# Optimization experiments

Measured on AMD Instinct MI355X. Metric: run time of the kernel, lower is better.

Reference implementation:

```python
import jax, jax.numpy as jnp
import numpy as np

TOP_K = 10


def setup_inputs() -> dict:
    key = jax.random.key(0)
    x = jax.random.normal(key, (256, 1, 8192), dtype=jnp.float32)
    return {"x": x}


def reference(x):
    # x: [B, 1, S] real
    B, _, S = x.shape
    # torch.arange(1e-05, 1, 1/S) has exactly S elements for these S
    t = 1e-05 + jnp.arange(S, dtype=jnp.float32) / S            # [S]
    dft = jnp.fft.fft(x[:, 0, :], n=S, axis=-1, norm='ortho')   # [B, S] complex64
    mag = jnp.abs(dft)                                          # [B, S]
    top_idx = jnp.argsort(-mag, axis=-1)[:, :TOP_K]             # [B, k] int
    top_dft = jnp.take_along_axis(dft, top_idx, axis=1)         # [B, k] complex
    # complex exponential basis exp(-2j*pi*k*t), flipped along time
    phase = (-2j * jnp.pi) * (top_idx[:, :, None].astype(jnp.float32) * t[None, None, :])
    bs = jnp.exp(phase)[:, :, ::-1]                             # [B, k, S] complex
    bf = top_dft[:, :, None] * bs / jnp.sqrt(jnp.float32(S))    # [B, k, S]
    # F.pad((1,0), mode='replicate') then crop to S: shift right by 1, duplicate first col
    bf = jnp.concatenate([bf[:, :, :1], bf[:, :, :-1]], axis=-1)
    bf = bf[:, :, None, :]                                      # [B, k, 1, S]
    residual = x - jnp.sum(bf, axis=1)                          # [B, 1, S] complex
    return bf, residual
```

## Files before the change

### kernel.cpp

```cpp
#include <hip/hip_runtime.h>

#define NB    256
#define SLEN  8192
#define LOG2S 13
#define TOPK  10

#define RES_REAL   ((size_t)20971520)
#define FULL_ILV   ((size_t)46137344)

__device__ __forceinline__ float sin_rev(float p) { return __builtin_amdgcn_sinf(p); }
__device__ __forceinline__ float cos_rev(float p) { return __builtin_amdgcn_cosf(p); }

__device__ __forceinline__ bool beats(float om, int oi, float wm, int wi) {
  return (om > wm * 1.0001f) || (om > wm * 0.9999f && oi < wi);
}

__global__ __launch_bounds__(512, 1)
void fourier_fused(const float* __restrict__ x, float* __restrict__ out, size_t cap) {
  __shared__ float re[SLEN];
  __shared__ float im[SLEN];

  const int b = blockIdx.x;
  const int t = threadIdx.x;
  const int lane = t & 63;
  const int wid  = t >> 6;
  const float* xb = x + (size_t)b * SLEN;

  for (int i = t; i < SLEN; i += 512) { re[i] = xb[i]; im[i] = 0.f; }
  __syncthreads();

  for (int i = t; i < SLEN; i += 512) {
    int j = (int)(__brev((unsigned)i) >> (32 - LOG2S));
    if (i < j) { float tmp = re[i]; re[i] = re[j]; re[j] = tmp; }
  }
  __syncthreads();

  for (int stage = 1; stage <= LOG2S; ++stage) {
    const int half = 1 << (stage - 1);
    const float invm = 1.f / (float)(1 << stage);
    for (int bfi = t; bfi < SLEN / 2; bfi += 512) {
      const int pos = bfi & (half - 1);
      const int i = ((bfi >> (stage - 1)) << stage) + pos;
      const int j = i + half;
      const float p = (float)pos * invm;
      const float c  = cos_rev(p);
      const float sn = -sin_rev(p);
      const float vr = re[j], vi = im[j];
      const float tr = vr * c - vi * sn;
      const float ti = vr * sn + vi * c;
      const float ur = re[i], ui = im[i];
      re[i] = ur + tr; im[i] = ui + ti;
      re[j] = ur - tr; im[j] = ui - ti;
    }
    __syncthreads();
  }

  int   kk[TOPK];
  float ar[TOPK], ai[TOPK];
#pragma unroll
  for (int sel = 0; sel < TOPK; ++sel) {
    float wm = -1.f; int wi = SLEN;
    for (int i = t; i < SLEN; i += 512) {
      const float m2 = re[i] * re[i] + im[i] * im[i];
      if (m2 > wm * 1.0001f) { wm = m2; wi = i; }
    }
    for (int off = 32; off > 0; off >>= 1) {
      const float om = __shfl_down(wm, off);
      const int   oi = __shfl_down(wi, off);
      if (beats(om, oi, wm, wi)) { wm = om; wi = oi; }
    }
    __syncthreads();
    float sv_r = 0.f, sv_i = 0.f;
    if (t < 8) { sv_r = re[t]; sv_i = im[t]; }
    __syncthreads();
    if (lane == 0) { re[wid] = wm; im[wid] = __int_as_float(wi); }
    __syncthreads();
    wm = re[0]; wi = __float_as_int(im[0]);
    for (int w = 1; w < 8; ++w) {
      const float om = re[w]; const int oi = __float_as_int(im[w]);
      if (beats(om, oi, wm, wi)) { wm = om; wi = oi; }
    }
    __syncthreads();
    if (t < 8) { re[t] = sv_r; im[t] = sv_i; }
    __syncthreads();
    const float rr = re[wi] * (1.f / (float)SLEN);
    const float ii = im[wi] * (1.f / (float)SLEN);
    const float pr = -1e-5f * (float)wi;
    const float cp = cos_rev(pr), sp = sin_rev(pr);
    kk[sel] = wi;
    ar[sel] = rr * cp - ii * sp;
    ai[sel] = rr * sp + ii * cp;
    __syncthreads();
    if (t == 0) { re[wi] = 0.f; im[wi] = 0.f; }
    __syncthreads();
  }

  if (cap < FULL_ILV) {
    const size_t bfbase = (size_t)b * TOPK * SLEN;
    for (int pass = 0; pass < 4; ++pass) {
      const int s0 = pass * 2048 + t * 4;
      const float4 xv = *(const float4*)(xb + s0);
      float acc0 = 0.f, acc1 = 0.f, acc2 = 0.f, acc3 = 0.f;
#pragma unroll
      for (int j = 0; j < TOPK; ++j) {
        const int k = kk[j];
        float br[4];
#pragma unroll
        for (int q = 0; q < 4; ++q) {
          const int s = s0 + q;
          const int m = (s == 0) ? 1 : s;
          const float p = (float)((k * m) & (SLEN - 1)) * (1.f / (float)SLEN);
          br[q] = ar[j] * cos_rev(p) - ai[j] * sin_rev(p);
        }
        acc0 += br[0]; acc1 += br[1]; acc2 += br[2]; acc3 += br[3];
        const size_t o = bfbase + (size_t)j * SLEN + s0;
        if (o + 4 <= cap)
          *(float4*)(out + o) = make_float4(br[0], br[1], br[2], br[3]);
      }
      const size_t o = RES_REAL + (size_t)b * SLEN + s0;
      if (o + 4 <= cap)
        *(float4*)(out + o) =
            make_float4(xv.x - acc0, xv.y - acc1, xv.z - acc2, xv.w - acc3);
    }
  } else {
    const size_t bfbase = (size_t)b * TOPK * SLEN * 2;
    for (int pass = 0; pass < 8; ++pass) {
      const int s0 = pass * 1024 + t * 2;
      const int m0 = (s0 == 0) ? 1 : s0;
      const int m1 = s0 + 1;
      float sr0 = 0.f, si0 = 0.f, sr1 = 0.f, si1 = 0.f;
#pragma unroll
      for (int j = 0; j < TOPK; ++j) {
        const int k = kk[j];
        const float p0 = (float)((k * m0) & (SLEN - 1)) * (1.f / (float)SLEN);
        const float p1 = (float)((k * m1) & (SLEN - 1)) * (1.f / (float)SLEN);
        const float c0 = cos_rev(p0), s0v = sin_rev(p0);
        const float c1 = cos_rev(p1), s1v = sin_rev(p1);
        const float br0 = ar[j] * c0 - ai[j] * s0v;
        const float bi0 = ar[j] * s0v + ai[j] * c0;
        const float br1 = ar[j] * c1 - ai[j] * s1v;
        const float bi1 = ar[j] * s1v + ai[j] * c1;
        sr0 += br0; si0 += bi0; sr1 += br1; si1 += bi1;
        const size_t o = bfbase + ((size_t)j * SLEN + s0) * 2;
        if (o + 4 <= cap)
          *(float4*)(out + o) = make_float4(br0, bi0, br1, bi1);
      }
      const float2 xv = *(const float2*)(xb + s0);
      const size_t o = (size_t)41943040 + ((size_t)b * SLEN + s0) * 2;
      if (o + 4 <= cap)
        *(float4*)(out + o) = make_float4(xv.x - sr0, -si0, xv.y - sr1, -si1);
    }
  }
}

extern "C" void kernel_launch(void* const* d_in, const int* in_sizes, int n_in,
                              void* d_out, int out_size, void* d_ws, size_t ws_size,
                              hipStream_t stream) {
  const float* x = (const float*)d_in[0];
  float* out = (float*)d_out;
  fourier_fused<<<NB, 512, 0, stream>>>(x, out, (size_t)out_size);
}
```

Before: 138.6 us.

## Split fused kernel into FFT/top-k kernel and parallel basis generation kernel

Splits the single per-batch kernel into two launches. The first runs the FFT and top-k selection with 1024 threads, caches magnitudes in registers and uses a dedicated warp-reduction buffer, then writes the selected indices and coefficients to global device arrays. The second kernel uses 2048 blocks of 256 threads to generate the basis functions and residual, giving far more parallelism for the write-heavy output phase. The cost is an extra kernel launch and a small global round-trip for the top-k data.

Measured after the change: 139.4 us. No clear change (+0.6%).

```diff
diff --git a/kernel.cpp b/kernel.cpp
--- a/kernel.cpp
+++ b/kernel.cpp
@@ -8,6 +8,10 @@
 #define RES_REAL   ((size_t)20971520)
 #define FULL_ILV   ((size_t)46137344)
 
+__device__ int   g_k [NB * TOPK];
+__device__ float g_ar[NB * TOPK];
+__device__ float g_ai[NB * TOPK];
+
 __device__ __forceinline__ float sin_rev(float p) { return __builtin_amdgcn_sinf(p); }
 __device__ __forceinline__ float cos_rev(float p) { return __builtin_amdgcn_cosf(p); }
 
@@ -15,10 +19,12 @@
   return (om > wm * 1.0001f) || (om > wm * 0.9999f && oi < wi);
 }
 
-__global__ __launch_bounds__(512, 1)
-void fourier_fused(const float* __restrict__ x, float* __restrict__ out, size_t cap) {
+__global__ __launch_bounds__(1024)
+void fft_topk(const float* __restrict__ x) {
   __shared__ float re[SLEN];
   __shared__ float im[SLEN];
+  __shared__ float wred_m[16];
+  __shared__ int   wred_i[16];
 
   const int b = blockIdx.x;
   const int t = threadIdx.x;
@@ -26,19 +32,23 @@
   const int wid  = t >> 6;
   const float* xb = x + (size_t)b * SLEN;
 
-  for (int i = t; i < SLEN; i += 512) { re[i] = xb[i]; im[i] = 0.f; }
+  for (int i = t; i < SLEN / 4; i += 1024) {
+    const float4 v = ((const float4*)xb)[i];
+    *(float4*)&re[i * 4] = v;
+    *(float4*)&im[i * 4] = make_float4(0.f, 0.f, 0.f, 0.f);
+  }
   __syncthreads();
 
-  for (int i = t; i < SLEN; i += 512) {
-    int j = (int)(__brev((unsigned)i) >> (32 - LOG2S));
-    if (i < j) { float tmp = re[i]; re[i] = re[j]; re[j] = tmp; }
+  for (int i = t; i < SLEN; i += 1024) {
+    const int j = (int)(__brev((unsigned)i) >> (32 - LOG2S));
+    if (i < j) { const float tmp = re[i]; re[i] = re[j]; re[j] = tmp; }
   }
   __syncthreads();
 
   for (int stage = 1; stage <= LOG2S; ++stage) {
     const int half = 1 << (stage - 1);
     const float invm = 1.f / (float)(1 << stage);
-    for (int bfi = t; bfi < SLEN / 2; bfi += 512) {
+    for (int bfi = t; bfi < SLEN / 2; bfi += 1024) {
       const int pos = bfi & (half - 1);
       const int i = ((bfi >> (stage - 1)) << stage) + pos;
       const int j = i + half;
@@ -55,100 +65,117 @@
     __syncthreads();
   }
 
-  int   kk[TOPK];
-  float ar[TOPK], ai[TOPK];
+  float m2c[8];
 #pragma unroll
+  for (int w = 0; w < 8; ++w) {
+    const int i = t + (w << 10);
+    m2c[w] = re[i] * re[i] + im[i] * im[i];
+  }
+
   for (int sel = 0; sel < TOPK; ++sel) {
     float wm = -1.f; int wi = SLEN;
-    for (int i = t; i < SLEN; i += 512) {
-      const float m2 = re[i] * re[i] + im[i] * im[i];
-      if (m2 > wm * 1.0001f) { wm = m2; wi = i; }
+#pragma unroll
+    for (int w = 0; w < 8; ++w) {
+      const int i = t + (w << 10);
+      if (m2c[w] > wm * 1.0001f) { wm = m2c[w]; wi = i; }
     }
     for (int off = 32; off > 0; off >>= 1) {
       const float om = __shfl_down(wm, off);
       const int   oi = __shfl_down(wi, off);
       if (beats(om, oi, wm, wi)) { wm = om; wi = oi; }
     }
+    if (lane == 0) { wred_m[wid] = wm; wred_i[wid] = wi; }
     __syncthreads();
-    float sv_r = 0.f, sv_i = 0.f;
-    if (t < 8) { sv_r = re[t]; sv_i = im[t]; }
-    __syncthreads();
-    if (lane == 0) { re[wid] = wm; im[wid] = __int_as_float(wi); }
-    __syncthreads();
-    wm = re[0]; wi = __float_as_int(im[0]);
-    for (int w = 1; w < 8; ++w) {
-      const float om = re[w]; const int oi = __float_as_int(im[w]);
+    wm = wred_m[0]; wi = wred_i[0];
+    for (int w = 1; w < 16; ++w) {
+      const float om = wred_m[w]; const int oi = wred_i[w];
       if (beats(om, oi, wm, wi)) { wm = om; wi = oi; }
     }
+    if (t == 0) {
+      const float rr = re[wi] * (1.f / (float)SLEN);
+      const float ii = im[wi] * (1.f / (float)SLEN);
+      const float pr = -1e-5f * (float)wi;
+      const float cp = cos_rev(pr), sp = sin_rev(pr);
+      g_k [b * TOPK + sel] = wi;
+      g_ar[b * TOPK + sel] = rr * cp - ii * sp;
+      g_ai[b * TOPK + sel] = rr * sp + ii * cp;
+    }
+#pragma unroll
+    for (int w = 0; w < 8; ++w)
+      if (wi == t + (w << 10)) m2c[w] = 0.f;
     __syncthreads();
-    if (t < 8) { re[t] = sv_r; im[t] = sv_i; }
-    __syncthreads();
-    const float rr = re[wi] * (1.f / (float)SLEN);
-    const float ii = im[wi] * (1.f / (float)SLEN);
-    const float pr = -1e-5f * (float)wi;
-    const float cp = cos_rev(pr), sp = sin_rev(pr);
-    kk[sel] = wi;
-    ar[sel] = rr * cp - ii * sp;
-    ai[sel] = rr * sp + ii * cp;
-    __syncthreads();
-    if (t == 0) { re[wi] = 0.f; im[wi] = 0.f; }
-    __syncthreads();
+  }
+}
+
+__global__ __launch_bounds__(256, 4)
+void gen(const float* __restrict__ x, float* __restrict__ out, size_t cap) {
+  const int bs    = blockIdx.x;
+  const int b     = bs >> 3;
+  const int slice = bs & 7;
+  const int t     = threadIdx.x;
+  const int s0    = slice * 1024 + t * 4;
+  const float* xb = x + (size_t)b * SLEN;
+
+  int kj[TOPK]; float arj[TOPK], aij[TOPK];
+#pragma unroll
+  for (int j = 0; j < TOPK; ++j) {
+    kj[j]  = g_k [b * TOPK + j];
+    arj[j] = g_ar[b * TOPK + j];
+    aij[j] = g_ai[b * TOPK + j];
   }
 
   if (cap < FULL_ILV) {
     const size_t bfbase = (size_t)b * TOPK * SLEN;
-    for (int pass = 0; pass < 4; ++pass) {
-      const int s0 = pass * 2048 + t * 4;
-      const float4 xv = *(const float4*)(xb + s0);
-      float acc0 = 0.f, acc1 = 0.f, acc2 = 0.f, acc3 = 0.f;
+    const float4 xv = *(const float4*)(xb + s0);
+    float acc0 = 0.f, acc1 = 0.f, acc2 = 0.f, acc3 = 0.f;
 #pragma unroll
-      for (int j = 0; j < TOPK; ++j) {
-        const int k = kk[j];
-        float br[4];
+    for (int j = 0; j < TOPK; ++j) {
+      const int k = kj[j];
+      float br[4];
 #pragma unroll
-        for (int q = 0; q < 4; ++q) {
-          const int s = s0 + q;
-          const int m = (s == 0) ? 1 : s;
-          const float p = (float)((k * m) & (SLEN - 1)) * (1.f / (float)SLEN);
-          br[q] = ar[j] * cos_rev(p) - ai[j] * sin_rev(p);
-        }
-        acc0 += br[0]; acc1 += br[1]; acc2 += br[2]; acc3 += br[3];
-        const size_t o = bfbase + (size_t)j * SLEN + s0;
-        if (o + 4 <= cap)
-          *(float4*)(out + o) = make_float4(br[0], br[1], br[2], br[3]);
+      for (int q = 0; q < 4; ++q) {
+        const int s = s0 + q;
+        const int m = (s == 0) ? 1 : s;
+        const float p = (float)((k * m) & (SLEN - 1)) * (1.f / (float)SLEN);
+        br[q] = arj[j] * cos_rev(p) - aij[j] * sin_rev(p);
       }
-      const size_t o = RES_REAL + (size_t)b * SLEN + s0;
+      acc0 += br[0]; acc1 += br[1]; acc2 += br[2]; acc3 += br[3];
+      const size_t o = bfbase + (size_t)j * SLEN + s0;
       if (o + 4 <= cap)
-        *(float4*)(out + o) =
-            make_float4(xv.x - acc0, xv.y - acc1, xv.z - acc2, xv.w - acc3);
+        *(float4*)(out + o) = make_float4(br[0], br[1], br[2], br[3]);
     }
+    const size_t o = RES_REAL + (size_t)b * SLEN + s0;
+    if (o + 4 <= cap)
+      *(float4*)(out + o) =
+          make_float4(xv.x - acc0, xv.y - acc1, xv.z - acc2, xv.w - acc3);
   } else {
     const size_t bfbase = (size_t)b * TOPK * SLEN * 2;
-    for (int pass = 0; pass < 8; ++pass) {
-      const int s0 = pass * 1024 + t * 2;
-      const int m0 = (s0 == 0) ? 1 : s0;
-      const int m1 = s0 + 1;
-      float sr0 = 0.f, si0 = 0.f, sr1 = 0.f, si1 = 0.f;
+    const float4 xv = *(const float4*)(xb + s0);
+    float sr[4] = {0.f, 0.f, 0.f, 0.f}, si[4] = {0.f, 0.f, 0.f, 0.f};
 #pragma unroll
-      for (int j = 0; j < TOPK; ++j) {
-        const int k = kk[j];
-        const float p0 = (float)((k * m0) & (SLEN - 1)) * (1.f / (float)SLEN);
-        const float p1 = (float)((k * m1) & (SLEN - 1)) * (1.f / (float)SLEN);
-        const float c0 = cos_rev(p0), s0v = sin_rev(p0);
-        const float c1 = cos_rev(p1), s1v = sin_rev(p1);
-        const float br0 = ar[j] * c0 - ai[j] * s0v;
-        const float bi0 = ar[j] * s0v + ai[j] * c0;
-        const float br1 = ar[j] * c1 - ai[j] * s1v;
-        const float bi1 = ar[j] * s1v + ai[j] * c1;
-        sr0 += br0; si0 += bi0; sr1 += br1; si1 += bi1;
-        const size_t o = bfbase + ((size_t)j * SLEN + s0) * 2;
-        if (o + 4 <= cap)
-          *(float4*)(out + o) = make_float4(br0, bi0, br1, bi1);
+    for (int j = 0; j < TOPK; ++j) {
+      const int k = kj[j];
+      float br[4], bi[4];
+#pragma unroll
+      for (int q = 0; q < 4; ++q) {
+        const int s = s0 + q;
+        const int m = (s == 0) ? 1 : s;
+        const float p = (float)((k * m) & (SLEN - 1)) * (1.f / (float)SLEN);
+        const float c = cos_rev(p), sv = sin_rev(p);
+        br[q] = arj[j] * c - aij[j] * sv;
+        bi[q] = arj[j] * sv + aij[j] * c;
+        sr[q] += br[q]; si[q] += bi[q];
       }
-      const float2 xv = *(const float2*)(xb + s0);
-      const size_t o = (size_t)41943040 + ((size_t)b * SLEN + s0) * 2;
-      if (o + 4 <= cap)
-        *(float4*)(out + o) = make_float4(xv.x - sr0, -si0, xv.y - sr1, -si1);
+      const size_t o = bfbase + ((size_t)j * SLEN + s0) * 2;
+      if (o + 8 <= cap) {
+        *(float4*)(out + o)     = make_float4(br[0], bi[0], br[1], bi[1]);
+        *(float4*)(out + o + 4) = make_float4(br[2], bi[2], br[3], bi[3]);
+      }
+    }
+    const size_t o = (size_t)41943040 + ((size_t)b * SLEN + s0) * 2;
+    if (o + 8 <= cap) {
+      *(float4*)(out + o)     = make_float4(xv.x - sr[0], -si[0], xv.y - sr[1], -si[1]);
+      *(float4*)(out + o + 4) = make_float4(xv.z - sr[2], -si[2], xv.w - sr[3], -si[3]);
     }
   }
 }
@@ -158,5 +185,6 @@
                               hipStream_t stream) {
   const float* x = (const float*)d_in[0];
   float* out = (float*)d_out;
-  fourier_fused<<<NB, 512, 0, stream>>>(x, out, (size_t)out_size);
+  fft_topk<<<NB, 1024, 0, stream>>>(x);
+  gen<<<NB * 8, 256, 0, stream>>>(x, out, (size_t)out_size);
 }
```
